# Kernel optimization log

Hardware: AMD Instinct MI355X
Metric: run time of the kernel (lower is better)

Reference implementation:

```python
import jax, jax.numpy as jnp
import numpy as np

LN_EPS = 1e-5
TOP_K = 2


def _layernorm(x):
    # parameter-free LayerNorm over last dim (elementwise_affine=False)
    mu = jnp.mean(x, axis=-1, keepdims=True)
    var = jnp.var(x, axis=-1, keepdims=True)
    return (x - mu) * jax.lax.rsqrt(var + LN_EPS)


def setup_inputs() -> dict:
    key = jax.random.key(0)
    k1, k2 = jax.random.split(key)
    inp = jax.random.normal(k1, (4, 4096, 2048), dtype=jnp.float32)
    emb = jax.random.normal(k2, (64, 2048), dtype=jnp.float32)
    return {"input": inp, "expert_embeddings": emb}


def reference(input, expert_embeddings):
    # standardize both the tokens and the expert embedding table
    x = _layernorm(input)                      # [b, s, d]
    e = _layernorm(expert_embeddings)          # [E, d]
    sim = jnp.einsum("bsd,ed->bse", x, e)      # [b, s, E]
    temp = jnp.sqrt(jnp.asarray(x.shape[-1], x.dtype))  # t=-1 -> sqrt(d)
    weights, module_indices = jax.lax.top_k(sim, TOP_K)  # [b, s, k]
    gates = jax.nn.softmax(weights / temp, axis=-1)
    return (module_indices, gates)
```

## Files before the change

### kernel.cpp

```cpp
#include <hip/hip_runtime.h>
#include <math.h>

#define D 2048
#define NE 64
#define NTOK 16384
#define KSPLIT 4
#define KRANGE (D / KSPLIT)
#define KSTEP 32
#define MTILE 128
#define LN_EPS 1e-5f
#define XSTRIDE (MTILE + 4)

__global__ __launch_bounds__(256) void expert_ln_kernel(
    const float* __restrict__ emb, float* __restrict__ eT) {
  const int e = blockIdx.x;
  const int tid = threadIdx.x;
  const float4* row = (const float4*)(emb + (size_t)e * D);
  float4 v0 = row[tid * 2];
  float4 v1 = row[tid * 2 + 1];
  float s = v0.x + v0.y + v0.z + v0.w + v1.x + v1.y + v1.z + v1.w;
  float q = v0.x * v0.x + v0.y * v0.y + v0.z * v0.z + v0.w * v0.w
          + v1.x * v1.x + v1.y * v1.y + v1.z * v1.z + v1.w * v1.w;
  #pragma unroll
  for (int off = 32; off > 0; off >>= 1) {
    s += __shfl_down(s, off);
    q += __shfl_down(q, off);
  }
  __shared__ float red[8];
  const int wid = tid >> 6;
  const int lane = tid & 63;
  if (lane == 0) { red[wid] = s; red[4 + wid] = q; }
  __syncthreads();
  if (tid == 0) {
    red[0] = red[0] + red[1] + red[2] + red[3];
    red[4] = red[4] + red[5] + red[6] + red[7];
  }
  __syncthreads();
  const float mu = red[0] * (1.0f / D);
  const float var = red[4] * (1.0f / D) - mu * mu;
  const float sc = rsqrtf(var + LN_EPS);
  float vals[8] = {v0.x, v0.y, v0.z, v0.w, v1.x, v1.y, v1.z, v1.w};
  const int k0 = tid * 8;
  #pragma unroll
  for (int j = 0; j < 8; ++j) {
    eT[(size_t)(k0 + j) * NE + e] = (vals[j] - mu) * sc;
  }
}

__global__ __launch_bounds__(256) void router_gemm_kernel(
    const float* __restrict__ x, const float* __restrict__ eT,
    float* __restrict__ dotP, float* __restrict__ sumP,
    float* __restrict__ sumsqP) {
  __shared__ float xT[KSTEP][XSTRIDE];
  __shared__ float eS[KSTEP][NE];
  const int tid = threadIdx.x;
  const int mt = blockIdx.x >> 2;
  const int kc = blockIdx.x & 3;
  const int K0 = kc * KRANGE;
  const int tr = tid >> 3;
  const int tc = tid & 7;
  const int ts = tid & 127;
  const int h = tid >> 7;

  float acc[4][8];
  #pragma unroll
  for (int i = 0; i < 4; ++i) {
    #pragma unroll
    for (int j = 0; j < 8; ++j) acc[i][j] = 0.0f;
  }
  float s1 = 0.0f, s2 = 0.0f;

  const float* xbase = x + (size_t)mt * MTILE * D + K0;

  for (int ck = 0; ck < KRANGE / KSTEP; ++ck) {
    const int kbase = ck * KSTEP;
    #pragma unroll
    for (int i = 0; i < 4; ++i) {
      const int idx = tid + i * 256;
      const int t = idx >> 3;
      const int kq = idx & 7;
      float4 v = *(const float4*)(xbase + (size_t)t * D + kbase + kq * 4);
      xT[kq * 4 + 0][t] = v.x;
      xT[kq * 4 + 1][t] = v.y;
      xT[kq * 4 + 2][t] = v.z;
      xT[kq * 4 + 3][t] = v.w;
    }
    #pragma unroll
    for (int i = 0; i < 2; ++i) {
      const int idx = tid + i * 256;
      *(float4*)&eS[0][idx * 4] =
          *(const float4*)(eT + (size_t)(K0 + kbase) * NE + (size_t)idx * 4);
    }
    __syncthreads();

    #pragma unroll
    for (int kk = 0; kk < 16; ++kk) {
      const float v = xT[h * 16 + kk][ts];
      s1 += v;
      s2 += v * v;
    }

    #pragma unroll 8
    for (int kk = 0; kk < KSTEP; ++kk) {
      float4 xv = *(const float4*)&xT[kk][tr * 4];
      float4 ea = *(const float4*)&eS[kk][tc * 8];
      float4 eb = *(const float4*)&eS[kk][tc * 8 + 4];
      float xr[4] = {xv.x, xv.y, xv.z, xv.w};
      float er[8] = {ea.x, ea.y, ea.z, ea.w, eb.x, eb.y, eb.z, eb.w};
      #pragma unroll
      for (int i = 0; i < 4; ++i) {
        #pragma unroll
        for (int j = 0; j < 8; ++j) {
          acc[i][j] = fmaf(xr[i], er[j], acc[i][j]);
        }
      }
    }
    __syncthreads();
  }

  float* red = &xT[0][0];
  red[h * 128 + ts] = s1;
  red[256 + h * 128 + ts] = s2;
  __syncthreads();
  if (tid < 128) {
    const int gt = mt * MTILE + tid;
    sumP[kc * NTOK + gt] = red[tid] + red[128 + tid];
    sumsqP[kc * NTOK + gt] = red[256 + tid] + red[384 + tid];
  }

  float* dp = dotP + ((size_t)kc * NTOK + (size_t)mt * MTILE) * NE;
  #pragma unroll
  for (int i = 0; i < 4; ++i) {
    const int t = tr * 4 + i;
    *(float4*)&dp[(size_t)t * NE + tc * 8] =
        make_float4(acc[i][0], acc[i][1], acc[i][2], acc[i][3]);
    *(float4*)&dp[(size_t)t * NE + tc * 8 + 4] =
        make_float4(acc[i][4], acc[i][5], acc[i][6], acc[i][7]);
  }
}

__global__ __launch_bounds__(256) void finalize_kernel(
    const float* __restrict__ dotP, const float* __restrict__ sumP,
    const float* __restrict__ sumsqP, float* __restrict__ out) {
  const int t = blockIdx.x * 256 + threadIdx.x;
  float s1 = 0.0f, s2 = 0.0f;
  #pragma unroll
  for (int kc = 0; kc < KSPLIT; ++kc) {
    s1 += sumP[kc * NTOK + t];
    s2 += sumsqP[kc * NTOK + t];
  }
  const float mu = s1 * (1.0f / D);
  const float var = s2 * (1.0f / D) - mu * mu;
  const float sc = rsqrtf(var + LN_EPS);

  float d[NE];
  #pragma unroll
  for (int e = 0; e < NE; ++e) d[e] = 0.0f;
  #pragma unroll
  for (int kc = 0; kc < KSPLIT; ++kc) {
    const float* dp = dotP + ((size_t)kc * NTOK + t) * NE;
    #pragma unroll
    for (int eq = 0; eq < NE / 4; ++eq) {
      float4 v = *(const float4*)&dp[eq * 4];
      d[eq * 4 + 0] += v.x;
      d[eq * 4 + 1] += v.y;
      d[eq * 4 + 2] += v.z;
      d[eq * 4 + 3] += v.w;
    }
  }

  float w1 = -INFINITY, w2 = -INFINITY;
  int i1 = 0, i2 = 0;
  #pragma unroll
  for (int e = 0; e < NE; ++e) {
    const float v = d[e] * sc;
    if (v > w1) {
      w2 = w1; i2 = i1; w1 = v; i1 = e;
    } else if (v > w2) {
      w2 = v; i2 = e;
    }
  }
  const float invT = 0.02209708691207961f;
  const float e1 = expf((w2 - w1) * invT);
  const float g1 = 1.0f / (1.0f + e1);
  const float g2 = e1 / (1.0f + e1);

  out[t * 2 + 0] = (float)i1;
  out[t * 2 + 1] = (float)i2;
  out[2 * NTOK + t * 2 + 0] = g1;
  out[2 * NTOK + t * 2 + 1] = g2;
}

extern "C" void kernel_launch(void* const* d_in, const int* in_sizes, int n_in,
                              void* d_out, int out_size, void* d_ws, size_t ws_size,
                              hipStream_t stream) {
  const float* x = (const float*)d_in[0];
  const float* emb = (const float*)d_in[1];
  float* ws = (float*)d_ws;
  float* eT = ws;
  float* dotP = ws + 131072;
  float* sumP = dotP + (size_t)KSPLIT * NTOK * NE;
  float* sumsqP = sumP + (size_t)KSPLIT * NTOK;
  float* out = (float*)d_out;

  expert_ln_kernel<<<NE, 256, 0, stream>>>(emb, eT);
  router_gemm_kernel<<<(NTOK / MTILE) * KSPLIT, 256, 0, stream>>>(
      x, eT, dotP, sumP, sumsqP);
  finalize_kernel<<<NTOK / 256, 256, 0, stream>>>(dotP, sumP, sumsqP, out);
}
```

Measured before the change: 233.0 us.

## Restructure router GEMM to stream expert rows from global and parallelize top-k finalize

The router GEMM now uses 64-token tiles with 64-wide K chunks. Each wave owns 16 experts and reads the normalized expert rows straight from global memory (wave-uniform, cache-resident) instead of staging them in LDS. Token sum and sum-of-squares are computed from registers during loading, and the block ordering groups blocks by K-split. The finalize kernel splits each token's 64 experts across 8 lanes and merges the top-2 results with xor shuffles, which improves coalescing and register pressure. The GEMM loses register-tile reuse (one x value per 16 FMAs, with global loads per k), which could limit throughput.

```diff
diff --git a/kernel.cpp b/kernel.cpp
--- a/kernel.cpp
+++ b/kernel.cpp
@@ -6,10 +6,11 @@
 #define NTOK 16384
 #define KSPLIT 4
 #define KRANGE (D / KSPLIT)
-#define KSTEP 32
-#define MTILE 128
+#define CHUNK 64
+#define NCHUNK (KRANGE / CHUNK)
+#define TBLK 64
+#define XSTRIDE 65
 #define LN_EPS 1e-5f
-#define XSTRIDE (MTILE + 4)
 
 __global__ __launch_bounds__(256) void expert_ln_kernel(
     const float* __restrict__ emb, float* __restrict__ eT) {
@@ -47,103 +48,97 @@
   }
 }
 
-__global__ __launch_bounds__(256) void router_gemm_kernel(
+__global__ __launch_bounds__(256, 4) void router_gemm_kernel(
     const float* __restrict__ x, const float* __restrict__ eT,
     float* __restrict__ dotP, float* __restrict__ sumP,
     float* __restrict__ sumsqP) {
-  __shared__ float xT[KSTEP][XSTRIDE];
-  __shared__ float eS[KSTEP][NE];
+  __shared__ float xT[CHUNK][XSTRIDE];
   const int tid = threadIdx.x;
-  const int mt = blockIdx.x >> 2;
-  const int kc = blockIdx.x & 3;
+  const int bt = blockIdx.x & 255;
+  const int kc = blockIdx.x >> 8;
   const int K0 = kc * KRANGE;
-  const int tr = tid >> 3;
-  const int tc = tid & 7;
-  const int ts = tid & 127;
-  const int h = tid >> 7;
-
-  float acc[4][8];
-  #pragma unroll
-  for (int i = 0; i < 4; ++i) {
+  const int lane = tid & 63;
+  const int wv = __builtin_amdgcn_readfirstlane(tid >> 6);
+  const int ts = tid >> 2;
+  const int kb = tid & 3;
+
+  float acc[16];
+  #pragma unroll
+  for (int j = 0; j < 16; ++j) acc[j] = 0.f;
+  float s1 = 0.f, s2 = 0.f;
+
+  const float* xrow = x + (size_t)(bt * TBLK + ts) * D + K0 + kb * 16;
+
+  for (int c = 0; c < NCHUNK; ++c) {
+    float4 v[4];
     #pragma unroll
-    for (int j = 0; j < 8; ++j) acc[i][j] = 0.0f;
-  }
-  float s1 = 0.0f, s2 = 0.0f;
-
-  const float* xbase = x + (size_t)mt * MTILE * D + K0;
-
-  for (int ck = 0; ck < KRANGE / KSTEP; ++ck) {
-    const int kbase = ck * KSTEP;
+    for (int j = 0; j < 4; ++j) v[j] = *(const float4*)(xrow + c * CHUNK + j * 4);
+    __syncthreads();
     #pragma unroll
-    for (int i = 0; i < 4; ++i) {
-      const int idx = tid + i * 256;
-      const int t = idx >> 3;
-      const int kq = idx & 7;
-      float4 v = *(const float4*)(xbase + (size_t)t * D + kbase + kq * 4);
-      xT[kq * 4 + 0][t] = v.x;
-      xT[kq * 4 + 1][t] = v.y;
-      xT[kq * 4 + 2][t] = v.z;
-      xT[kq * 4 + 3][t] = v.w;
-    }
-    #pragma unroll
-    for (int i = 0; i < 2; ++i) {
-      const int idx = tid + i * 256;
-      *(float4*)&eS[0][idx * 4] =
-          *(const float4*)(eT + (size_t)(K0 + kbase) * NE + (size_t)idx * 4);
+    for (int j = 0; j < 4; ++j) {
+      s1 += v[j].x + v[j].y + v[j].z + v[j].w;
+      s2 += v[j].x * v[j].x + v[j].y * v[j].y + v[j].z * v[j].z + v[j].w * v[j].w;
+      const int kr = kb * 16 + j * 4;
+      xT[kr + 0][ts] = v[j].x;
+      xT[kr + 1][ts] = v[j].y;
+      xT[kr + 2][ts] = v[j].z;
+      xT[kr + 3][ts] = v[j].w;
     }
     __syncthreads();
-
-    #pragma unroll
-    for (int kk = 0; kk < 16; ++kk) {
-      const float v = xT[h * 16 + kk][ts];
-      s1 += v;
-      s2 += v * v;
+    const float* ep = eT + (size_t)(K0 + c * CHUNK) * NE + wv * 16;
+    #pragma unroll 4
+    for (int kk = 0; kk < CHUNK; ++kk) {
+      const float xv = xT[kk][lane];
+      const float4 e0 = *(const float4*)(ep + (size_t)kk * NE + 0);
+      const float4 e1 = *(const float4*)(ep + (size_t)kk * NE + 4);
+      const float4 e2 = *(const float4*)(ep + (size_t)kk * NE + 8);
+      const float4 e3 = *(const float4*)(ep + (size_t)kk * NE + 12);
+      acc[0]  = fmaf(e0.x, xv, acc[0]);
+      acc[1]  = fmaf(e0.y, xv, acc[1]);
+      acc[2]  = fmaf(e0.z, xv, acc[2]);
+      acc[3]  = fmaf(e0.w, xv, acc[3]);
+      acc[4]  = fmaf(e1.x, xv, acc[4]);
+      acc[5]  = fmaf(e1.y, xv, acc[5]);
+      acc[6]  = fmaf(e1.z, xv, acc[6]);
+      acc[7]  = fmaf(e1.w, xv, acc[7]);
+      acc[8]  = fmaf(e2.x, xv, acc[8]);
+      acc[9]  = fmaf(e2.y, xv, acc[9]);
+      acc[10] = fmaf(e2.z, xv, acc[10]);
+      acc[11] = fmaf(e2.w, xv, acc[11]);
+      acc[12] = fmaf(e3.x, xv, acc[12]);
+      acc[13] = fmaf(e3.y, xv, acc[13]);
+      acc[14] = fmaf(e3.z, xv, acc[14]);
+      acc[15] = fmaf(e3.w, xv, acc[15]);
     }
-
-    #pragma unroll 8
-    for (int kk = 0; kk < KSTEP; ++kk) {
-      float4 xv = *(const float4*)&xT[kk][tr * 4];
-      float4 ea = *(const float4*)&eS[kk][tc * 8];
-      float4 eb = *(const float4*)&eS[kk][tc * 8 + 4];
-      float xr[4] = {xv.x, xv.y, xv.z, xv.w};
-      float er[8] = {ea.x, ea.y, ea.z, ea.w, eb.x, eb.y, eb.z, eb.w};
-      #pragma unroll
-      for (int i = 0; i < 4; ++i) {
-        #pragma unroll
-        for (int j = 0; j < 8; ++j) {
-          acc[i][j] = fmaf(xr[i], er[j], acc[i][j]);
-        }
-      }
-    }
-    __syncthreads();
-  }
-
+  }
+
+  __syncthreads();
   float* red = &xT[0][0];
-  red[h * 128 + ts] = s1;
-  red[256 + h * 128 + ts] = s2;
-  __syncthreads();
-  if (tid < 128) {
-    const int gt = mt * MTILE + tid;
-    sumP[kc * NTOK + gt] = red[tid] + red[128 + tid];
-    sumsqP[kc * NTOK + gt] = red[256 + tid] + red[384 + tid];
-  }
-
-  float* dp = dotP + ((size_t)kc * NTOK + (size_t)mt * MTILE) * NE;
-  #pragma unroll
-  for (int i = 0; i < 4; ++i) {
-    const int t = tr * 4 + i;
-    *(float4*)&dp[(size_t)t * NE + tc * 8] =
-        make_float4(acc[i][0], acc[i][1], acc[i][2], acc[i][3]);
-    *(float4*)&dp[(size_t)t * NE + tc * 8 + 4] =
-        make_float4(acc[i][4], acc[i][5], acc[i][6], acc[i][7]);
-  }
+  red[kb * 64 + ts] = s1;
+  red[256 + kb * 64 + ts] = s2;
+  __syncthreads();
+  if (tid < TBLK) {
+    const int gt = bt * TBLK + tid;
+    sumP[kc * NTOK + gt] = red[tid] + red[64 + tid] + red[128 + tid] + red[192 + tid];
+    sumsqP[kc * NTOK + gt] =
+        red[256 + tid] + red[320 + tid] + red[384 + tid] + red[448 + tid];
+  }
+
+  float* dp = dotP + ((size_t)kc * NTOK + (size_t)bt * TBLK + lane) * NE + wv * 16;
+  *(float4*)(dp + 0)  = make_float4(acc[0], acc[1], acc[2], acc[3]);
+  *(float4*)(dp + 4)  = make_float4(acc[4], acc[5], acc[6], acc[7]);
+  *(float4*)(dp + 8)  = make_float4(acc[8], acc[9], acc[10], acc[11]);
+  *(float4*)(dp + 12) = make_float4(acc[12], acc[13], acc[14], acc[15]);
 }
 
 __global__ __launch_bounds__(256) void finalize_kernel(
     const float* __restrict__ dotP, const float* __restrict__ sumP,
     const float* __restrict__ sumsqP, float* __restrict__ out) {
-  const int t = blockIdx.x * 256 + threadIdx.x;
-  float s1 = 0.0f, s2 = 0.0f;
+  const int tid = threadIdx.x;
+  const int t = blockIdx.x * 32 + (tid >> 3);
+  const int l8 = tid & 7;
+
+  float s1 = 0.f, s2 = 0.f;
   #pragma unroll
   for (int kc = 0; kc < KSPLIT; ++kc) {
     s1 += sumP[kc * NTOK + t];
@@ -153,42 +148,51 @@
   const float var = s2 * (1.0f / D) - mu * mu;
   const float sc = rsqrtf(var + LN_EPS);
 
-  float d[NE];
-  #pragma unroll
-  for (int e = 0; e < NE; ++e) d[e] = 0.0f;
+  float d[8] = {0.f, 0.f, 0.f, 0.f, 0.f, 0.f, 0.f, 0.f};
   #pragma unroll
   for (int kc = 0; kc < KSPLIT; ++kc) {
-    const float* dp = dotP + ((size_t)kc * NTOK + t) * NE;
-    #pragma unroll
-    for (int eq = 0; eq < NE / 4; ++eq) {
-      float4 v = *(const float4*)&dp[eq * 4];
-      d[eq * 4 + 0] += v.x;
-      d[eq * 4 + 1] += v.y;
-      d[eq * 4 + 2] += v.z;
-      d[eq * 4 + 3] += v.w;
-    }
+    const float* dp = dotP + ((size_t)kc * NTOK + t) * NE + l8 * 8;
+    float4 a = *(const float4*)dp;
+    float4 b = *(const float4*)(dp + 4);
+    d[0] += a.x; d[1] += a.y; d[2] += a.z; d[3] += a.w;
+    d[4] += b.x; d[5] += b.y; d[6] += b.z; d[7] += b.w;
   }
 
   float w1 = -INFINITY, w2 = -INFINITY;
   int i1 = 0, i2 = 0;
   #pragma unroll
-  for (int e = 0; e < NE; ++e) {
-    const float v = d[e] * sc;
-    if (v > w1) {
-      w2 = w1; i2 = i1; w1 = v; i1 = e;
-    } else if (v > w2) {
-      w2 = v; i2 = e;
+  for (int j = 0; j < 8; ++j) {
+    const float v = d[j] * sc;
+    const int e = l8 * 8 + j;
+    if (v > w1) { w2 = w1; i2 = i1; w1 = v; i1 = e; }
+    else if (v > w2) { w2 = v; i2 = e; }
+  }
+  #pragma unroll
+  for (int off = 1; off < 8; off <<= 1) {
+    const float ow1 = __shfl_xor(w1, off);
+    const float ow2 = __shfl_xor(w2, off);
+    const int oi1 = __shfl_xor(i1, off);
+    const int oi2 = __shfl_xor(i2, off);
+    if (ow1 > w1 || (ow1 == w1 && oi1 < i1)) {
+      float nw2; int ni2;
+      if (w1 > ow2 || (w1 == ow2 && i1 < oi2)) { nw2 = w1; ni2 = i1; }
+      else { nw2 = ow2; ni2 = oi2; }
+      w1 = ow1; i1 = oi1; w2 = nw2; i2 = ni2;
+    } else {
+      if (ow1 > w2 || (ow1 == w2 && oi1 < i2)) { w2 = ow1; i2 = oi1; }
     }
   }
-  const float invT = 0.02209708691207961f;
-  const float e1 = expf((w2 - w1) * invT);
-  const float g1 = 1.0f / (1.0f + e1);
-  const float g2 = e1 / (1.0f + e1);
-
-  out[t * 2 + 0] = (float)i1;
-  out[t * 2 + 1] = (float)i2;
-  out[2 * NTOK + t * 2 + 0] = g1;
-  out[2 * NTOK + t * 2 + 1] = g2;
+
+  if (l8 == 0) {
+    const float invT = 0.02209708691207961f;
+    const float e1 = expf((w2 - w1) * invT);
+    const float g1 = 1.0f / (1.0f + e1);
+    const float g2 = e1 * g1;
+    out[t * 2 + 0] = (float)i1;
+    out[t * 2 + 1] = (float)i2;
+    out[2 * NTOK + t * 2 + 0] = g1;
+    out[2 * NTOK + t * 2 + 1] = g2;
+  }
 }
 
 extern "C" void kernel_launch(void* const* d_in, const int* in_sizes, int n_in,
@@ -204,7 +208,7 @@
   float* out = (float*)d_out;
 
   expert_ln_kernel<<<NE, 256, 0, stream>>>(emb, eT);
-  router_gemm_kernel<<<(NTOK / MTILE) * KSPLIT, 256, 0, stream>>>(
+  router_gemm_kernel<<<KSPLIT * (NTOK / TBLK), 256, 0, stream>>>(
       x, eT, dotP, sumP, sumsqP);
-  finalize_kernel<<<NTOK / 256, 256, 0, stream>>>(dotP, sumP, sumsqP, out);
-}
+  finalize_kernel<<<NTOK / 32, 256, 0, stream>>>(dotP, sumP, sumsqP, out);
+}
```

Result: slower. 262.6 us (+12.7%).
